# Kernel tuning notes

Hardware: AMD Instinct MI355X
Metric: run time of the kernel (lower is better)

The kernel has to match this reference:

```python
import jax, jax.numpy as jnp
import numpy as np

THRESHOLD = 0.05


def ternary_project(w, threshold=THRESHOLD, use_ste=True):
    # scale: mean |w| over all axes except the last (per-output-column scale)
    reduce_axes = tuple(range(w.ndim - 1))
    scale = jnp.mean(jnp.abs(w), axis=reduce_axes, keepdims=True)
    ternary = jnp.where(jnp.abs(w) < threshold, 0.0, jnp.sign(w)) * scale
    if use_ste:
        return w + jax.lax.stop_gradient(ternary - w)
    return ternary


def setup_inputs() -> dict:
    key = jax.random.key(0)
    kx, kw = jax.random.split(key)
    B, S, D, O = 8, 2048, 4096, 4096
    x = jax.random.normal(kx, (B, S, D), dtype=jnp.float32)
    w = jax.random.normal(kw, (D, O), dtype=jnp.float32) * 0.02  # small init like VarianceScaling
    b = jnp.zeros((O,), dtype=jnp.float32)
    return {"x": x, "w": w, "b": b}


def reference(x, w, b):
    y = x @ ternary_project(w, threshold=THRESHOLD, use_ste=True)
    return y + b
```

## Files before the change

kernel.cpp:

```cpp
#include <hip/hip_runtime.h>
#include <stdint.h>

typedef int i32x4 __attribute__((ext_vector_type(4)));

#define D_DIM 4096
#define O_DIM 4096
#define M_DIM 16384
#define THRESH 0.05f


__device__ __forceinline__ void gld16(const void* g, void* l) {
  __builtin_amdgcn_global_load_lds(
      (const __attribute__((address_space(1))) uint32_t*)(uintptr_t)g,
      (__attribute__((address_space(3))) uint32_t*)(uint32_t)(uintptr_t)l,
      16, 0, 0);
}

__device__ __forceinline__ int tern_i8(float v) {
  return (__builtin_fabsf(v) < THRESH) ? 0 : (v > 0.f ? 1 : -1);
}


__global__ void k_scale_part(const float* __restrict__ w, float* __restrict__ part) {
  const int cg = blockIdx.x & 63;
  const int dz = blockIdx.x >> 6;
  const int tx = threadIdx.x & 63;
  const int ty = threadIdx.x >> 6;
  const int o = cg * 64 + tx;
  float s = 0.f;
  const float* p = w + (size_t)(dz * 512 + ty) * O_DIM + o;
  for (int i = 0; i < 128; ++i) {
    s += __builtin_fabsf(*p);
    p += 4 * O_DIM;
  }
  __shared__ float red[4][64];
  red[ty][tx] = s;
  __syncthreads();
  if (ty == 0) part[dz * O_DIM + o] = (red[0][tx] + red[1][tx]) + (red[2][tx] + red[3][tx]);
}

__global__ void k_scale_fin(const float* __restrict__ part, float* __restrict__ scale) {
  const int o = blockIdx.x * 256 + threadIdx.x;
  float s = 0.f;
#pragma unroll
  for (int z = 0; z < 8; ++z) s += part[z * O_DIM + o];
  scale[o] = s * (1.0f / 4096.0f);
}

__global__ void k_tern_q(const float* __restrict__ w, char* __restrict__ btq) {
  __shared__ char tile[64][68];
  const int ot = blockIdx.x & 63;
  const int dt = blockIdx.x >> 6;
  const int o0 = ot * 64, d0 = dt * 64;
  const int tx = threadIdx.x & 15, ty = threadIdx.x >> 4;
#pragma unroll
  for (int j = 0; j < 4; ++j) {
    const int r = ty + 16 * j;
    const float4 v = *(const float4*)&w[(size_t)(d0 + r) * O_DIM + o0 + tx * 4];
    uint32_t u = (uint32_t)(tern_i8(v.x) & 0xFF) |
                 ((uint32_t)(tern_i8(v.y) & 0xFF) << 8) |
                 ((uint32_t)(tern_i8(v.z) & 0xFF) << 16) |
                 ((uint32_t)(tern_i8(v.w) & 0xFF) << 24);
    *(uint32_t*)&tile[r][tx * 4] = u;
  }
  __syncthreads();
#pragma unroll
  for (int j = 0; j < 4; ++j) {
    const int orow = ty + 16 * j;
    uint32_t u = (uint32_t)((uint8_t)tile[tx * 4 + 0][orow]) |
                 ((uint32_t)((uint8_t)tile[tx * 4 + 1][orow]) << 8) |
                 ((uint32_t)((uint8_t)tile[tx * 4 + 2][orow]) << 16) |
                 ((uint32_t)((uint8_t)tile[tx * 4 + 3][orow]) << 24);
    *(uint32_t*)&btq[(size_t)(o0 + orow) * D_DIM + d0 + tx * 4] = u;
  }
}

__global__ void k_quant(const float* __restrict__ x, char* __restrict__ xq,
                        float* __restrict__ sx) {
  const int row = blockIdx.x;
  const int t = threadIdx.x;
  const float* xr = x + (size_t)row * D_DIM + t * 16;
  float4 v[4];
#pragma unroll
  for (int i = 0; i < 4; ++i) v[i] = *(const float4*)(xr + i * 4);
  float m = 0.f;
#pragma unroll
  for (int i = 0; i < 4; ++i) {
    m = fmaxf(m, fmaxf(fmaxf(__builtin_fabsf(v[i].x), __builtin_fabsf(v[i].y)),
                       fmaxf(__builtin_fabsf(v[i].z), __builtin_fabsf(v[i].w))));
  }
#pragma unroll
  for (int off = 32; off >= 1; off >>= 1) m = fmaxf(m, __shfl_xor(m, off, 64));
  __shared__ float wm[4];
  if ((t & 63) == 0) wm[t >> 6] = m;
  __syncthreads();
  const float rm = fmaxf(fmaxf(wm[0], wm[1]), fmaxf(wm[2], wm[3]));
  const float inv = (rm > 0.f) ? 127.0f / rm : 0.0f;
  int4 o;
  int* op = (int*)&o;
#pragma unroll
  for (int i = 0; i < 4; ++i) {
    const float* f = (const float*)&v[i];
    uint32_t u = 0;
#pragma unroll
    for (int j = 0; j < 4; ++j) {
      float q = __builtin_rintf(f[j] * inv);
      q = fmaxf(-127.f, fminf(127.f, q));
      u |= ((uint32_t)((int)q & 0xFF)) << (8 * j);
    }
    op[i] = (int)u;
  }
  *(int4*)(xq + (size_t)row * D_DIM + t * 16) = o;
  if (t == 0) sx[row] = (rm > 0.f) ? rm * (1.0f / 127.0f) : 0.0f;
}


#define BAR() __builtin_amdgcn_s_barrier()
#define SB0() __builtin_amdgcn_sched_barrier(0)
#define LGKM(n) asm volatile("s_waitcnt lgkmcnt(" #n ")" ::: "memory")
#define VMW(n) asm volatile("s_waitcnt vmcnt(" #n ")" ::: "memory")

#define STAGE_A(d, kv)                                              \
  do {                                                              \
    gld16(pA0 + (size_t)(kv) * 128, smem + (d)*16384 + t * 16);     \
    gld16(pA1 + (size_t)(kv) * 128, smem + (d)*16384 + 4096 + t * 16); \
    gld16(pA2 + (size_t)(kv) * 128, smem + (d)*16384 + 8192 + t * 16); \
    gld16(pA3 + (size_t)(kv) * 128, smem + (d)*16384 + 12288 + t * 16); \
  } while (0)
#define STAGE_B(d, kv)                                              \
  do {                                                              \
    gld16(pB0 + (size_t)(kv) * 128, smem + 32768 + (d)*16384 + t * 16); \
    gld16(pB1 + (size_t)(kv) * 128, smem + 32768 + (d)*16384 + 4096 + t * 16); \
    gld16(pB2 + (size_t)(kv) * 128, smem + 32768 + (d)*16384 + 8192 + t * 16); \
    gld16(pB3 + (size_t)(kv) * 128, smem + 32768 + (d)*16384 + 12288 + t * 16); \
  } while (0)

#define RA(d)                                                          \
  do {                                                                 \
    const char* ab_ = smem + (d)*16384 + (wr * 64 + r16) * 128;        \
    _Pragma("unroll") for (int m4 = 0; m4 < 4; ++m4) {                 \
      aq[0][m4] = *(const i32x4*)(ab_ + m4 * 2048 + slot0);            \
      aq[1][m4] = *(const i32x4*)(ab_ + m4 * 2048 + (slot0 ^ 64));     \
    }                                                                  \
  } while (0)
#define RB(db)                                                         \
  do {                                                                 \
    const char* bb_ = smem + 32768 + (db)*16384 + (wc * 64 + r16) * 128; \
    _Pragma("unroll") for (int n4 = 0; n4 < 4; ++n4) {                 \
      bq[0][n4] = *(const i32x4*)(bb_ + n4 * 2048 + slot0);            \
      bq[1][n4] = *(const i32x4*)(bb_ + n4 * 2048 + (slot0 ^ 64));     \
    }                                                                  \
  } while (0)

#define MQ(kk)                                                                \
  do {                                                                        \
    __builtin_amdgcn_s_setprio(1);                                            \
    _Pragma("unroll") for (int m4 = 0; m4 < 4; ++m4)                          \
    _Pragma("unroll") for (int n4 = 0; n4 < 4; ++n4)                          \
        acc[m4][n4] = __builtin_amdgcn_mfma_i32_16x16x64_i8(                  \
            aq[kk][m4], bq[kk][n4], acc[m4][n4], 0, 0, 0);                    \
    __builtin_amdgcn_s_setprio(0);                                            \
  } while (0)

#define TILE(d, kv)                                                      \
  do {                                                                   \
    RA(d);                                                               \
    STAGE_B(d, kv);                                                      \
    BAR(); LGKM(4); SB0();                                               \
    MQ(0);                                                               \
    BAR();                                                               \
    STAGE_A(d, kv);                                                      \
    LGKM(0); SB0();                                                      \
    MQ(1);                                                               \
    VMW(8); BAR();                                                       \
    RB((d) ^ 1); SB0();                                                  \
    BAR();                                                               \
  } while (0)

__global__ __launch_bounds__(256, 2) void k_gemm8(
    const char* __restrict__ A,
    const char* __restrict__ B,
    const float* __restrict__ sx, const float* __restrict__ scale,
    const float* __restrict__ bias, float* __restrict__ C) {
  __shared__ __align__(16) char smem[65536];

  const int bid = blockIdx.x;
  const int xcd = bid & 7, s = bid >> 3;
  const int nb = xcd * 4 + (s & 3);
  const int mb = s >> 2;
  const int mBase = mb * 128, nBase = nb * 128;

  const int t = threadIdx.x;
  const int lane = t & 63, wid = t >> 6;
  const int wr = wid >> 1, wc = wid & 1;
  const int r16 = lane & 15, kq = lane >> 4;
  const int slot0 = (kq ^ (r16 & 7)) << 4;

  const int sr0 = t >> 3, sg0 = (t & 7) ^ (sr0 & 7);
  const int q1 = 256 + t, q2 = 512 + t, q3 = 768 + t;
  const int sr1 = q1 >> 3, sg1 = (q1 & 7) ^ (sr1 & 7);
  const int sr2 = q2 >> 3, sg2 = (q2 & 7) ^ (sr2 & 7);
  const int sr3 = q3 >> 3, sg3 = (q3 & 7) ^ (sr3 & 7);

  const char* pA0 = A + (size_t)(mBase + sr0) * D_DIM + sg0 * 16;
  const char* pA1 = A + (size_t)(mBase + sr1) * D_DIM + sg1 * 16;
  const char* pA2 = A + (size_t)(mBase + sr2) * D_DIM + sg2 * 16;
  const char* pA3 = A + (size_t)(mBase + sr3) * D_DIM + sg3 * 16;
  const char* pB0 = B + (size_t)(nBase + sr0) * D_DIM + sg0 * 16;
  const char* pB1 = B + (size_t)(nBase + sr1) * D_DIM + sg1 * 16;
  const char* pB2 = B + (size_t)(nBase + sr2) * D_DIM + sg2 * 16;
  const char* pB3 = B + (size_t)(nBase + sr3) * D_DIM + sg3 * 16;

  i32x4 acc[4][4] = {};
  i32x4 aq[2][4];
  i32x4 bq[2][4];

  STAGE_A(0, 0); STAGE_B(0, 0);
  STAGE_A(1, 1); STAGE_B(1, 1);
  VMW(8);
  BAR();
  RB(0);
  BAR();

  for (int T = 0; T < 32; T += 2) {
    TILE(0, (T + 2) & 31);
    TILE(1, (T + 3) & 31);
  }
  VMW(0);

  float sxr[4][4];
#pragma unroll
  for (int mi = 0; mi < 4; ++mi) {
    const int gr0 = mBase + wr * 64 + mi * 16 + kq * 4;
#pragma unroll
    for (int r = 0; r < 4; ++r) sxr[mi][r] = sx[gr0 + r];
  }
#pragma unroll
  for (int ni = 0; ni < 4; ++ni) {
    const int gc = nBase + wc * 64 + ni * 16 + r16;
    const float sw = scale[gc];
    const float bb = bias[gc];
#pragma unroll
    for (int mi = 0; mi < 4; ++mi) {
      const int gr0 = mBase + wr * 64 + mi * 16 + kq * 4;
#pragma unroll
      for (int r = 0; r < 4; ++r) {
        __builtin_nontemporal_store(
            (float)acc[mi][ni][r] * (sxr[mi][r] * sw) + bb,
            &C[(size_t)(gr0 + r) * O_DIM + gc]);
      }
    }
  }
}


extern "C" void kernel_launch(void* const* d_in, const int* in_sizes, int n_in,
                              void* d_out, int out_size, void* d_ws, size_t ws_size,
                              hipStream_t stream) {
  const float* x = (const float*)d_in[0];
  const float* w = (const float*)d_in[1];
  const float* bias = (const float*)d_in[2];
  float* out = (float*)d_out;

  const size_t XQ_OFF = 0;
  const size_t BT_OFF = (size_t)M_DIM * D_DIM;
  const size_t SX_OFF = BT_OFF + (size_t)O_DIM * D_DIM;
  const size_t PART_OFF = SX_OFF + (size_t)M_DIM * 4;
  const size_t SCALE_OFF = PART_OFF + 8 * O_DIM * 4;
  const size_t NEED = SCALE_OFF + O_DIM * 4;
  if (ws_size < NEED) return;

  char* ws = (char*)d_ws;
  char* xq = ws + XQ_OFF;
  char* btq = ws + BT_OFF;
  float* sx = (float*)(ws + SX_OFF);
  float* part = (float*)(ws + PART_OFF);
  float* scale = (float*)(ws + SCALE_OFF);

  k_scale_part<<<512, 256, 0, stream>>>(w, part);
  k_scale_fin<<<16, 256, 0, stream>>>(part, scale);
  k_tern_q<<<64 * 64, 256, 0, stream>>>(w, btq);
  k_quant<<<M_DIM, 256, 0, stream>>>(x, xq, sx);
  k_gemm8<<<4096, 256, 0, stream>>>(xq, btq, sx, scale, bias, out);
}
```

Baseline: 327.9 us.

## Restructure GEMM tile pipeline to read all LDS fragments before restaging

Each tile iteration now reads both A and B fragments for the current buffer from LDS up front, then issues one barrier and stages the next A and B tiles together. Previously B was prefetched from the other buffer at the end of the tile. This cuts the barriers per tile from four to two and lets the first MFMA batch start after waiting only on the k0 half of the LDS reads. The cost is that B fragments are no longer read early, so LDS read latency sits closer to the MFMAs, and more fragment registers are live at once.

Measured after the change: 319.0 us (median of 2 runs). 2.7% less time.

```diff
diff --git a/kernel.cpp b/kernel.cpp
--- a/kernel.cpp
+++ b/kernel.cpp
@@ -135,21 +135,29 @@
     gld16(pB3 + (size_t)(kv) * 128, smem + 32768 + (d)*16384 + 12288 + t * 16); \
   } while (0)
 
-#define RA(d)                                                          \
+#define RA0(d)                                                         \
   do {                                                                 \
     const char* ab_ = smem + (d)*16384 + (wr * 64 + r16) * 128;        \
-    _Pragma("unroll") for (int m4 = 0; m4 < 4; ++m4) {                 \
-      aq[0][m4] = *(const i32x4*)(ab_ + m4 * 2048 + slot0);            \
-      aq[1][m4] = *(const i32x4*)(ab_ + m4 * 2048 + (slot0 ^ 64));     \
-    }                                                                  \
-  } while (0)
-#define RB(db)                                                         \
-  do {                                                                 \
-    const char* bb_ = smem + 32768 + (db)*16384 + (wc * 64 + r16) * 128; \
-    _Pragma("unroll") for (int n4 = 0; n4 < 4; ++n4) {                 \
-      bq[0][n4] = *(const i32x4*)(bb_ + n4 * 2048 + slot0);            \
-      bq[1][n4] = *(const i32x4*)(bb_ + n4 * 2048 + (slot0 ^ 64));     \
-    }                                                                  \
+    _Pragma("unroll") for (int m4 = 0; m4 < 4; ++m4)                   \
+        aq[0][m4] = *(const i32x4*)(ab_ + m4 * 2048 + slot0);          \
+  } while (0)
+#define RA1(d)                                                         \
+  do {                                                                 \
+    const char* ab_ = smem + (d)*16384 + (wr * 64 + r16) * 128;        \
+    _Pragma("unroll") for (int m4 = 0; m4 < 4; ++m4)                   \
+        aq[1][m4] = *(const i32x4*)(ab_ + m4 * 2048 + (slot0 ^ 64));   \
+  } while (0)
+#define RB0(d)                                                         \
+  do {                                                                 \
+    const char* bb_ = smem + 32768 + (d)*16384 + (wc * 64 + r16) * 128; \
+    _Pragma("unroll") for (int n4 = 0; n4 < 4; ++n4)                   \
+        bq[0][n4] = *(const i32x4*)(bb_ + n4 * 2048 + slot0);          \
+  } while (0)
+#define RB1(d)                                                         \
+  do {                                                                 \
+    const char* bb_ = smem + 32768 + (d)*16384 + (wc * 64 + r16) * 128; \
+    _Pragma("unroll") for (int n4 = 0; n4 < 4; ++n4)                   \
+        bq[1][n4] = *(const i32x4*)(bb_ + n4 * 2048 + (slot0 ^ 64));   \
   } while (0)
 
 #define MQ(kk)                                                                \
@@ -164,17 +172,15 @@
 
 #define TILE(d, kv)                                                      \
   do {                                                                   \
-    RA(d);                                                               \
-    STAGE_B(d, kv);                                                      \
-    BAR(); LGKM(4); SB0();                                               \
+    RA0(d); RB0(d);                                                      \
+    RA1(d); RB1(d);                                                      \
+    BAR();                                                               \
+    STAGE_A(d, kv); STAGE_B(d, kv);                                      \
+    LGKM(8); SB0();                                                      \
     MQ(0);                                                               \
-    BAR();                                                               \
-    STAGE_A(d, kv);                                                      \
     LGKM(0); SB0();                                                      \
     MQ(1);                                                               \
     VMW(8); BAR();                                                       \
-    RB((d) ^ 1); SB0();                                                  \
-    BAR();                                                               \
   } while (0)
 
 __global__ __launch_bounds__(256, 2) void k_gemm8(
@@ -219,8 +225,6 @@
   STAGE_A(1, 1); STAGE_B(1, 1);
   VMW(8);
   BAR();
-  RB(0);
-  BAR();
 
   for (int T = 0; T < 32; T += 2) {
     TILE(0, (T + 2) & 31);
```

## Load A operand directly from global into registers, keep only B in LDS

Applied to the files above, without the earlier changes.

The A tile is no longer staged through LDS. Each wave loads its A fragments straight from global memory into double-buffered registers, one k-tile ahead. This halves LDS use to 32 KB and cuts the LDS write and read traffic for A, which could allow more occupancy and less LDS bandwidth pressure. In exchange, loads for A are no longer shared across waves, since waves in the same row each fetch the same data. The direct loads are less coalesced 16-byte accesses, and the extra registers for the second A buffer may increase register pressure.

Result: slower. 636.7 us (+94.2%).

```diff
diff --git a/kernel.cpp b/kernel.cpp
--- a/kernel.cpp
+++ b/kernel.cpp
@@ -120,60 +120,60 @@
 #define LGKM(n) asm volatile("s_waitcnt lgkmcnt(" #n ")" ::: "memory")
 #define VMW(n) asm volatile("s_waitcnt vmcnt(" #n ")" ::: "memory")
 
-#define STAGE_A(d, kv)                                              \
-  do {                                                              \
-    gld16(pA0 + (size_t)(kv) * 128, smem + (d)*16384 + t * 16);     \
-    gld16(pA1 + (size_t)(kv) * 128, smem + (d)*16384 + 4096 + t * 16); \
-    gld16(pA2 + (size_t)(kv) * 128, smem + (d)*16384 + 8192 + t * 16); \
-    gld16(pA3 + (size_t)(kv) * 128, smem + (d)*16384 + 12288 + t * 16); \
-  } while (0)
-#define STAGE_B(d, kv)                                              \
-  do {                                                              \
-    gld16(pB0 + (size_t)(kv) * 128, smem + 32768 + (d)*16384 + t * 16); \
-    gld16(pB1 + (size_t)(kv) * 128, smem + 32768 + (d)*16384 + 4096 + t * 16); \
-    gld16(pB2 + (size_t)(kv) * 128, smem + 32768 + (d)*16384 + 8192 + t * 16); \
-    gld16(pB3 + (size_t)(kv) * 128, smem + 32768 + (d)*16384 + 12288 + t * 16); \
-  } while (0)
-
-#define RA(d)                                                          \
-  do {                                                                 \
-    const char* ab_ = smem + (d)*16384 + (wr * 64 + r16) * 128;        \
-    _Pragma("unroll") for (int m4 = 0; m4 < 4; ++m4) {                 \
-      aq[0][m4] = *(const i32x4*)(ab_ + m4 * 2048 + slot0);            \
-      aq[1][m4] = *(const i32x4*)(ab_ + m4 * 2048 + (slot0 ^ 64));     \
-    }                                                                  \
-  } while (0)
-#define RB(db)                                                         \
-  do {                                                                 \
-    const char* bb_ = smem + 32768 + (db)*16384 + (wc * 64 + r16) * 128; \
-    _Pragma("unroll") for (int n4 = 0; n4 < 4; ++n4) {                 \
-      bq[0][n4] = *(const i32x4*)(bb_ + n4 * 2048 + slot0);            \
-      bq[1][n4] = *(const i32x4*)(bb_ + n4 * 2048 + (slot0 ^ 64));     \
-    }                                                                  \
-  } while (0)
-
-#define MQ(kk)                                                                \
+#define STAGE_B(d, kv)                                                  \
+  do {                                                                  \
+    gld16(pB0 + (size_t)(kv) * 128, smem + (d)*16384 + t * 16);         \
+    gld16(pB1 + (size_t)(kv) * 128, smem + (d)*16384 + 4096 + t * 16);  \
+    gld16(pB2 + (size_t)(kv) * 128, smem + (d)*16384 + 8192 + t * 16);  \
+    gld16(pB3 + (size_t)(kv) * 128, smem + (d)*16384 + 12288 + t * 16); \
+  } while (0)
+
+#define RB0(d)                                                           \
+  do {                                                                   \
+    const char* bb_ = smem + (d)*16384 + (wc * 64 + r16) * 128;          \
+    _Pragma("unroll") for (int n4 = 0; n4 < 4; ++n4)                     \
+        bq[0][n4] = *(const i32x4*)(bb_ + n4 * 2048 + slot0);            \
+  } while (0)
+#define RB1(d)                                                           \
+  do {                                                                   \
+    const char* bb_ = smem + (d)*16384 + (wc * 64 + r16) * 128;          \
+    _Pragma("unroll") for (int n4 = 0; n4 < 4; ++n4)                     \
+        bq[1][n4] = *(const i32x4*)(bb_ + n4 * 2048 + (slot0 ^ 64));     \
+  } while (0)
+
+#define LOADA(AQ, kv)                                                    \
+  do {                                                                   \
+    const size_t ko_ = (size_t)(kv) * 128;                               \
+    AQ[0][0] = *(const i32x4*)(pAg0 + ko_);                              \
+    AQ[1][0] = *(const i32x4*)(pAg0 + ko_ + 64);                         \
+    AQ[0][1] = *(const i32x4*)(pAg1 + ko_);                              \
+    AQ[1][1] = *(const i32x4*)(pAg1 + ko_ + 64);                         \
+    AQ[0][2] = *(const i32x4*)(pAg2 + ko_);                              \
+    AQ[1][2] = *(const i32x4*)(pAg2 + ko_ + 64);                         \
+    AQ[0][3] = *(const i32x4*)(pAg3 + ko_);                              \
+    AQ[1][3] = *(const i32x4*)(pAg3 + ko_ + 64);                         \
+  } while (0)
+
+#define MQ(kk, AC)                                                            \
   do {                                                                        \
     __builtin_amdgcn_s_setprio(1);                                            \
     _Pragma("unroll") for (int m4 = 0; m4 < 4; ++m4)                          \
     _Pragma("unroll") for (int n4 = 0; n4 < 4; ++n4)                          \
         acc[m4][n4] = __builtin_amdgcn_mfma_i32_16x16x64_i8(                  \
-            aq[kk][m4], bq[kk][n4], acc[m4][n4], 0, 0, 0);                    \
+            AC[kk][m4], bq[kk][n4], acc[m4][n4], 0, 0, 0);                    \
     __builtin_amdgcn_s_setprio(0);                                            \
   } while (0)
 
-#define TILE(d, kv)                                                      \
-  do {                                                                   \
-    RA(d);                                                               \
-    STAGE_B(d, kv);                                                      \
-    BAR(); LGKM(4); SB0();                                               \
-    MQ(0);                                                               \
+#define TILE(d, AC, AN, Tv)                                              \
+  do {                                                                   \
+    RB0(d); RB1(d);                                                      \
     BAR();                                                               \
-    STAGE_A(d, kv);                                                      \
+    STAGE_B(d, ((Tv) + 2) & 31);                                         \
+    LOADA(AN, ((Tv) + 1) & 31);                                          \
+    VMW(12); LGKM(4); SB0();                                             \
+    MQ(0, AC);                                                           \
     LGKM(0); SB0();                                                      \
-    MQ(1);                                                               \
-    VMW(8); BAR();                                                       \
-    RB((d) ^ 1); SB0();                                                  \
+    MQ(1, AC);                                                           \
     BAR();                                                               \
   } while (0)
 
@@ -182,7 +182,7 @@
     const char* __restrict__ B,
     const float* __restrict__ sx, const float* __restrict__ scale,
     const float* __restrict__ bias, float* __restrict__ C) {
-  __shared__ __align__(16) char smem[65536];
+  __shared__ __align__(16) char smem[32768];
 
   const int bid = blockIdx.x;
   const int xcd = bid & 7, s = bid >> 3;
@@ -202,29 +202,29 @@
   const int sr2 = q2 >> 3, sg2 = (q2 & 7) ^ (sr2 & 7);
   const int sr3 = q3 >> 3, sg3 = (q3 & 7) ^ (sr3 & 7);
 
-  const char* pA0 = A + (size_t)(mBase + sr0) * D_DIM + sg0 * 16;
-  const char* pA1 = A + (size_t)(mBase + sr1) * D_DIM + sg1 * 16;
-  const char* pA2 = A + (size_t)(mBase + sr2) * D_DIM + sg2 * 16;
-  const char* pA3 = A + (size_t)(mBase + sr3) * D_DIM + sg3 * 16;
   const char* pB0 = B + (size_t)(nBase + sr0) * D_DIM + sg0 * 16;
   const char* pB1 = B + (size_t)(nBase + sr1) * D_DIM + sg1 * 16;
   const char* pB2 = B + (size_t)(nBase + sr2) * D_DIM + sg2 * 16;
   const char* pB3 = B + (size_t)(nBase + sr3) * D_DIM + sg3 * 16;
 
+  const char* pAg0 = A + (size_t)(mBase + wr * 64 + 0 * 16 + r16) * D_DIM + kq * 16;
+  const char* pAg1 = A + (size_t)(mBase + wr * 64 + 1 * 16 + r16) * D_DIM + kq * 16;
+  const char* pAg2 = A + (size_t)(mBase + wr * 64 + 2 * 16 + r16) * D_DIM + kq * 16;
+  const char* pAg3 = A + (size_t)(mBase + wr * 64 + 3 * 16 + r16) * D_DIM + kq * 16;
+
   i32x4 acc[4][4] = {};
-  i32x4 aq[2][4];
+  i32x4 aqA[2][4], aqB[2][4];
   i32x4 bq[2][4];
 
-  STAGE_A(0, 0); STAGE_B(0, 0);
-  STAGE_A(1, 1); STAGE_B(1, 1);
+  STAGE_B(0, 0);
+  STAGE_B(1, 1);
+  LOADA(aqA, 0);
   VMW(8);
   BAR();
-  RB(0);
-  BAR();
 
   for (int T = 0; T < 32; T += 2) {
-    TILE(0, (T + 2) & 31);
-    TILE(1, (T + 3) & 31);
+    TILE(0, aqA, aqB, T);
+    TILE(1, aqB, aqA, T + 1);
   }
   VMW(0);
 
```
